# Optimization experiments

Measured on AMD Instinct MI355X. Metric: run time of the kernel, lower is better.

The kernel has to match this reference:

```python
import jax, jax.numpy as jnp
import numpy as np

N = 50000   # nodes
E = 800000  # edges (avg degree 16)
NEG = 0.2   # leaky_relu negative slope


def gat_conv(feat, W, al, ar, rW, src, dst, act):
    """DGL-style GATConv. feat:[N,F] W:[F,H*D] al/ar:[H,D] rW:[F,H*D] or None (identity residual)."""
    n = feat.shape[0]
    H, D = al.shape
    h = (feat @ W).reshape(n, H, D)                      # [N,H,D]
    el = jnp.einsum('nhd,hd->nh', h, al)                 # [N,H]
    er = jnp.einsum('nhd,hd->nh', h, ar)                 # [N,H]
    e = el[src] + er[dst]                                # [E,H]
    e = jnp.where(e > 0, e, NEG * e)                     # leaky_relu
    emax = jax.ops.segment_max(e, dst, num_segments=n)   # per-dst softmax (edge softmax)
    ee = jnp.exp(e - emax[dst])
    denom = jax.ops.segment_sum(ee, dst, num_segments=n)
    alpha = ee / denom[dst]                              # [E,H]
    out = jax.ops.segment_sum(h[src] * alpha[:, :, None], dst, num_segments=n)  # [N,H,D]
    res = (feat @ rW).reshape(n, H, D) if rW is not None else feat.reshape(n, H, D)
    return act(out + res)


def setup_inputs() -> dict:
    key = jax.random.key(0)
    ks = jax.random.split(key, 32)
    d = {}
    d["fvs"] = jax.random.normal(ks[0], (N, 128), jnp.float32)
    d["pos_enc"] = jax.random.normal(ks[1], (N, 64), jnp.float32)
    d["src"] = jax.random.randint(ks[2], (E,), 0, N, jnp.int32)
    d["dst"] = jax.random.randint(ks[3], (E,), 0, N, jnp.int32)
    def w(k, shape):
        return jax.random.normal(k, shape, jnp.float32) / np.sqrt(shape[0])
    i = 4
    # gat layers: in=192 -> H=2, D=64 (layers 0,1), final: H=2, D=64 (out_ch)
    for name in ["gat0", "gat1", "gat2"]:
        d[name + "_W"] = w(ks[i], (192, 128)); i += 1
        d[name + "_al"] = w(ks[i], (2, 64)); i += 1
        d[name + "_ar"] = w(ks[i], (2, 64)); i += 1
        d[name + "_rW"] = w(ks[i], (192, 128)); i += 1
    # pgnn layers: in=64 -> H=2, D=32; in == H*D so residual is identity (no rW)
    for name in ["pg0", "pg1"]:
        d[name + "_W"] = w(ks[i], (64, 64)); i += 1
        d[name + "_al"] = w(ks[i], (2, 32)); i += 1
        d[name + "_ar"] = w(ks[i], (2, 32)); i += 1
    return d


def reference(fvs, pos_enc, src, dst,
              gat0_W, gat0_al, gat0_ar, gat0_rW,
              gat1_W, gat1_al, gat1_ar, gat1_rW,
              gat2_W, gat2_al, gat2_ar, gat2_rW,
              pg0_W, pg0_al, pg0_ar,
              pg1_W, pg1_al, pg1_ar):
    n = fvs.shape[0]
    h_s, h_p = fvs, pos_enc
    # layer 0
    h_s = jnp.concatenate([h_s, h_p], axis=1)
    h_s = gat_conv(h_s, gat0_W, gat0_al, gat0_ar, gat0_rW, src, dst, jax.nn.elu).reshape(n, -1)
    h_p = gat_conv(h_p, pg0_W, pg0_al, pg0_ar, None, src, dst, jnp.tanh).reshape(n, -1)
    # layer 1
    h_s = jnp.concatenate([h_s, h_p], axis=1)
    h_s = gat_conv(h_s, gat1_W, gat1_al, gat1_ar, gat1_rW, src, dst, jax.nn.elu).reshape(n, -1)
    h_p = gat_conv(h_p, pg1_W, pg1_al, pg1_ar, None, src, dst, jnp.tanh).reshape(n, -1)
    # output layer: mean over heads
    h_s = jnp.concatenate([h_s, h_p], axis=1)
    h_s = gat_conv(h_s, gat2_W, gat2_al, gat2_ar, gat2_rW, src, dst, jax.nn.elu).mean(axis=1)
    return (h_s, h_p)
```

## Files before the change

### kernel.cpp

```cpp
#include <hip/hip_runtime.h>

#define NN 50000
#define NE 800000

typedef unsigned short u16;
typedef unsigned int u32;

typedef float f32x4 __attribute__((ext_vector_type(4)));
typedef __bf16 bf16x8 __attribute__((ext_vector_type(8)));
static_assert(sizeof(bf16x8) == 16, "bf16x8 must be 16B");

__device__ __forceinline__ float bf2f(u16 u) {
    u32 x = ((u32)u) << 16;
    return __uint_as_float(x);
}
__device__ __forceinline__ u16 f2bf(float f) {
    u32 x = __float_as_uint(f);
    u32 r = (x + 0x7fffu + ((x >> 16) & 1u)) >> 16;
    return (u16)r;
}
__device__ __forceinline__ u32 pack2(float a, float b) {
    return (u32)f2bf(a) | ((u32)f2bf(b) << 16);
}
__device__ __forceinline__ u16 f2h(float f) {
    _Float16 h = (_Float16)f;
    union { _Float16 h; u16 u; } c; c.h = h;
    return c.u;
}
__device__ __forceinline__ float h2f(u16 u) {
    union { u16 u; _Float16 h; } c; c.u = u;
    return (float)c.h;
}
__device__ __forceinline__ uint4 packu4(const u16* h) {
    uint4 u;
    u.x = (u32)h[0] | ((u32)h[1] << 16);
    u.y = (u32)h[2] | ((u32)h[3] << 16);
    u.z = (u32)h[4] | ((u32)h[5] << 16);
    u.w = (u32)h[6] | ((u32)h[7] << 16);
    return u;
}
__device__ __forceinline__ float ldf(const void* p, size_t idx, int mode) {
    return mode ? bf2f(((const u16*)p)[idx]) : ((const float*)p)[idx];
}
__device__ __forceinline__ float lrelu(float x) { return x > 0.f ? x : 0.2f * x; }

__device__ __forceinline__ f32x4 mfma16(uint4 a, uint4 b, f32x4 c) {
    union { uint4 u; bf16x8 b; } ua, ub;
    ua.u = a; ub.u = b;
    return __builtin_amdgcn_mfma_f32_16x16x32_bf16(ua.b, ub.b, c, 0, 0, 0);
}

__global__ void k_tracer(float* out, float v) {
    if (threadIdx.x == 0 && blockIdx.x == 0) out[0] = v;
}

__global__ void k_detect(const u16* __restrict__ fvs, int* __restrict__ mode) {
    __shared__ int cnt[256];
    int t = threadIdx.x;
    int bad = 0;
    for (int i = 0; i < 16; i++) {
        u16 u = fvs[(size_t)(t * 16 + i) * 2];
        int e = (u >> 7) & 0xff;
        if (e == 255 || e >= 134 || e <= 100) bad++;
    }
    cnt[t] = bad;
    __syncthreads();
    for (int d = 128; d; d >>= 1) {
        if (t < d) cnt[t] += cnt[t + d];
        __syncthreads();
    }
    if (t == 0) *mode = (cnt[0] > 2048) ? 0 : 1;
}

__global__ void k_hist(const int* __restrict__ dst, int* __restrict__ cnt, int E) {
    int e = blockIdx.x * blockDim.x + threadIdx.x;
    if (e < E) atomicAdd(&cnt[dst[e]], 1);
}

__global__ void k_scan1(const int* __restrict__ cnt, int* __restrict__ off,
                        int* __restrict__ bsum, int N) {
    __shared__ int wsum[4];
    int t = threadIdx.x;
    int base = blockIdx.x * 2048 + t * 8;
    int e[8];
    if (base + 8 <= N) {
        int4 v0 = *(const int4*)&cnt[base];
        int4 v1 = *(const int4*)&cnt[base + 4];
        e[0] = v0.x; e[1] = v0.y; e[2] = v0.z; e[3] = v0.w;
        e[4] = v1.x; e[5] = v1.y; e[6] = v1.z; e[7] = v1.w;
    } else {
#pragma unroll
        for (int i = 0; i < 8; i++) e[i] = (base + i < N) ? cnt[base + i] : 0;
    }
    int s = 0;
    int ps[8];
#pragma unroll
    for (int i = 0; i < 8; i++) { ps[i] = s; s += e[i]; }
    int lane = t & 63, wv = t >> 6;
    int sc = s;
#pragma unroll
    for (int o = 1; o < 64; o <<= 1) {
        int u = __shfl_up(sc, o, 64);
        if (lane >= o) sc += u;
    }
    if (lane == 63) wsum[wv] = sc;
    __syncthreads();
    int woff = 0;
    for (int w = 0; w < wv; w++) woff += wsum[w];
    int ex = woff + sc - s;
#pragma unroll
    for (int i = 0; i < 8; i++) ps[i] += ex;
    if (base + 8 <= N) {
        *(int4*)&off[base] = make_int4(ps[0], ps[1], ps[2], ps[3]);
        *(int4*)&off[base + 4] = make_int4(ps[4], ps[5], ps[6], ps[7]);
    } else {
#pragma unroll
        for (int i = 0; i < 8; i++)
            if (base + i < N) off[base + i] = ps[i];
    }
    if (t == 255) bsum[blockIdx.x] = woff + sc;
}

__global__ void k_scan2(const int* __restrict__ bsum, int* __restrict__ off,
                        int N, int nb) {
    int b = blockIdx.x, t = threadIdx.x;
    int boff = 0;
    for (int i = 0; i < b; i++) boff += bsum[i];
    int base = b * 2048 + t * 8;
    if (b > 0) {
        if (base + 8 <= N) {
            int4 a = *(int4*)&off[base];
            int4 c = *(int4*)&off[base + 4];
            a.x += boff; a.y += boff; a.z += boff; a.w += boff;
            c.x += boff; c.y += boff; c.z += boff; c.w += boff;
            *(int4*)&off[base] = a;
            *(int4*)&off[base + 4] = c;
        } else {
#pragma unroll
            for (int i = 0; i < 8; i++)
                if (base + i < N) off[base + i] += boff;
        }
    }
    if (b == nb - 1 && t == 255) off[N] = boff + bsum[b];
}

__global__ void k_fill(const int* __restrict__ src, const int* __restrict__ dst,
                       const int* __restrict__ off, int* __restrict__ cnt2,
                       int* __restrict__ ssrc, int E) {
    int e = blockIdx.x * blockDim.x + threadIdx.x;
    if (e < E) {
        int d = dst[e];
        int p = off[d] + atomicAdd(&cnt2[d], 1);
        ssrc[p] = src[e];
    }
}

__global__ void k_init(const void* __restrict__ pos, u16* __restrict__ hp,
                       const int* __restrict__ dmode, int n64) {
    int i = blockIdx.x * blockDim.x + threadIdx.x;
    if (i >= n64) return;
    int mode = *dmode;
    hp[i] = mode ? ((const u16*)pos)[i] : f2bf(((const float*)pos)[i]);
}

__global__ void k_cvt(const u16* __restrict__ in, float* __restrict__ out, int n) {
    int i = blockIdx.x * blockDim.x + threadIdx.x;
    if (i < n) out[i] = bf2f(in[i]);
}

struct PWArgs {
    const void* src[8];
    u16* dst[8];
    int K[8];
    int BM[8];
};

__global__ void k_prepw(PWArgs a, const int* __restrict__ dmode) {
    int mode = *dmode;
    int g = blockIdx.x * blockDim.x + threadIdx.x;
    int stride = gridDim.x * blockDim.x;
    for (int m = 0; m < 8; m++) {
        int bm = a.BM[m];
        int bmsh = (bm == 128) ? 7 : 6;
        int n = a.K[m] * bm;
        u16* d = a.dst[m];
        const void* s = a.src[m];
        for (int i = g; i < n; i += stride) {
            int k = i >> bmsh, c = i & (bm - 1);
            float v = mode ? bf2f(((const u16*)s)[i]) : ((const float*)s)[i];
            u16 hi = f2bf(v);
            u16 lo = f2bf(v - bf2f(hi));
            size_t o = ((size_t)((k >> 5) * 2) * bm + c) * 32 + (k & 31);
            d[o] = hi;
            d[o + (size_t)bm * 32] = lo;
        }
    }
}

template <int BM, bool HASB2, bool C1H>
__launch_bounds__(256, 4)
__global__ void k_gemm(const void* A1, const u16* __restrict__ A2,
                       const u16* __restrict__ B1p, const u16* __restrict__ B2p,
                       void* __restrict__ C1, u16* C2, float* __restrict__ att,
                       const void* __restrict__ al, const void* __restrict__ ar,
                       int N, int K, int s1, const int* __restrict__ dmode,
                       int a1_input) {
    constexpr int NR = BM / 32;
    constexpr int NMAT = HASB2 ? 2 : 1;

    const int mode = *dmode;
    const int a1f32 = (a1_input && mode == 0) ? 1 : 0;
    const int bsplit = (mode == 0) ? 1 : 0;

    const int tid = threadIdx.x;
    const int lane = tid & 63;
    const int wid = tid >> 6;
    const int l15 = lane & 15, l4 = lane >> 4;
    const int r0 = blockIdx.x * 64;
    const int wrow0 = (wid >> 1) * 32;
    const int wcol0 = (wid & 1) * (BM / 2);
    const int ko = l4 * 8;

    int frow[2];
#pragma unroll
    for (int m = 0; m < 2; m++) {
        int r = r0 + wrow0 + m * 16 + l15;
        frow[m] = r < N ? r : N - 1;
    }

    f32x4 acc[NMAT][2][NR];
    const f32x4 fz = {0.f, 0.f, 0.f, 0.f};
#pragma unroll
    for (int m2 = 0; m2 < NMAT; m2++)
#pragma unroll
        for (int m = 0; m < 2; m++)
#pragma unroll
            for (int n = 0; n < NR; n++) acc[m2][m][n] = fz;

    const int NKT = K >> 5;
    for (int kt = 0; kt < NKT; kt++) {
        const int k0 = kt << 5;
        const int doAlo = (a1f32 && k0 < 128) ? 1 : 0;

        uint4 ah[2], alo[2];
#pragma unroll
        for (int m = 0; m < 2; m++) {
            if (k0 >= 128) {
                ah[m] = *(const uint4*)(A2 + (size_t)frow[m] * 64 + (k0 - 128) + ko);
            } else if (!a1f32) {
                ah[m] = *(const uint4*)((const u16*)A1 + (size_t)frow[m] * s1 + k0 + ko);
            } else {
                const float* p = (const float*)A1 + (size_t)frow[m] * s1 + k0 + ko;
                union { uint4 u[2]; float f[8]; } fa;
                fa.u[0] = *(const uint4*)p;
                fa.u[1] = *(const uint4*)(p + 4);
                u16 hi[8], lo[8];
#pragma unroll
                for (int i = 0; i < 8; i++) {
                    hi[i] = f2bf(fa.f[i]);
                    lo[i] = f2bf(fa.f[i] - bf2f(hi[i]));
                }
                ah[m] = packu4(hi);
                alo[m] = packu4(lo);
            }
        }

        const size_t bbase = ((size_t)kt * 2) * BM * 32 + (size_t)l4 * 8;
#pragma unroll
        for (int n = 0; n < NR; n++) {
            const int c = wcol0 + n * 16 + l15;
            const size_t co = (size_t)c * 32;
#pragma unroll
            for (int m2 = 0; m2 < NMAT; m2++) {
                const u16* bp = (m2 == 0 ? B1p : B2p) + bbase + co;
                uint4 bh = *(const uint4*)bp;
#pragma unroll
                for (int m = 0; m < 2; m++)
                    acc[m2][m][n] = mfma16(ah[m], bh, acc[m2][m][n]);
                if (bsplit) {
                    uint4 bl = *(const uint4*)(bp + (size_t)BM * 32);
#pragma unroll
                    for (int m = 0; m < 2; m++)
                        acc[m2][m][n] = mfma16(ah[m], bl, acc[m2][m][n]);
                }
                if (doAlo) {
#pragma unroll
                    for (int m = 0; m < 2; m++)
                        acc[m2][m][n] = mfma16(alo[m], bh, acc[m2][m][n]);
                }
            }
        }
    }

    __syncthreads();

    float alc[NR], arc[NR];
#pragma unroll
    for (int n = 0; n < NR; n++) {
        int c = wcol0 + n * 16 + l15;
        alc[n] = ldf(al, c, mode);
        arc[n] = ldf(ar, c, mode);
    }
    const int hc = wid & 1;
#pragma unroll
    for (int m = 0; m < 2; m++) {
#pragma unroll
        for (int r = 0; r < 4; r++) {
            const int gr = r0 + wrow0 + m * 16 + l4 * 4 + r;
            float el = 0.f, er = 0.f;
#pragma unroll
            for (int n = 0; n < NR; n++) {
                float v = acc[0][m][n][r];
                el = fmaf(v, alc[n], el);
                er = fmaf(v, arc[n], er);
            }
#pragma unroll
            for (int o = 1; o <= 8; o <<= 1) {
                el += __shfl_xor(el, o, 64);
                er += __shfl_xor(er, o, 64);
            }
            if (gr < N) {
#pragma unroll
                for (int n = 0; n < NR; n++) {
                    const int c = wcol0 + n * 16 + l15;
                    float v = acc[0][m][n][r];
                    if constexpr (C1H)
                        ((u16*)C1)[(size_t)gr * BM + c] = f2h(v);
                    else
                        ((float*)C1)[(size_t)gr * BM + c] = v;
                    if constexpr (HASB2)
                        C2[(size_t)gr * 128 + c] = f2bf(acc[1][m][n][r]);
                }
                if (l15 == 0) {
                    att[(size_t)gr * 4 + hc] = el;
                    att[(size_t)gr * 4 + 2 + hc] = er;
                }
            }
        }
    }
}

__global__ void k_edge_gat2(const int* __restrict__ off, const int* __restrict__ ssrc,
                            const u16* __restrict__ h, const float* __restrict__ att,
                            const u16* __restrict__ res, u16* __restrict__ outf, int N) {
    __shared__ float pbuf[4][2][64];
    __shared__ int sbuf[4][64];
    int wv = threadIdx.x >> 6;
    int node = blockIdx.x * 4 + wv;
    int lane = threadIdx.x & 63;
    if (node >= N) return;
    const int hd = lane >> 5;
    int beg = off[node], end = off[node + 1];
    float4 a4 = *(const float4*)&att[(size_t)node * 4];
    float er0 = a4.z, er1 = a4.w;
    float m0 = -1e30f, m1 = -1e30f, d0 = 0.f, d1 = 0.f, O0 = 0.f, O1 = 0.f;
    for (int c = beg; c < end; c += 64) {
        int cn = min(end - c, 64);
        int s = 0;
        float x0 = -1e30f, x1 = -1e30f;
        if (lane < cn) {
            s = ssrc[c + lane];
            float2 e = *(const float2*)&att[(size_t)s * 4];
            x0 = lrelu(e.x + er0);
            x1 = lrelu(e.y + er1);
        }
        float cm0 = x0, cm1 = x1;
#pragma unroll
        for (int o = 32; o; o >>= 1) {
            cm0 = fmaxf(cm0, __shfl_xor(cm0, o, 64));
            cm1 = fmaxf(cm1, __shfl_xor(cm1, o, 64));
        }
        float nm0 = fmaxf(m0, cm0), nm1 = fmaxf(m1, cm1);
        float p0 = (lane < cn) ? __expf(x0 - nm0) : 0.f;
        float p1 = (lane < cn) ? __expf(x1 - nm1) : 0.f;
        float cd0 = p0, cd1 = p1;
#pragma unroll
        for (int o = 32; o; o >>= 1) {
            cd0 += __shfl_xor(cd0, o, 64);
            cd1 += __shfl_xor(cd1, o, 64);
        }
        float sc0 = __expf(m0 - nm0), sc1 = __expf(m1 - nm1);
        d0 = d0 * sc0 + cd0; d1 = d1 * sc1 + cd1;
        float sch = hd ? sc1 : sc0;
        O0 *= sch; O1 *= sch;
        m0 = nm0; m1 = nm1;
        pbuf[wv][0][lane] = p0;
        pbuf[wv][1][lane] = p1;
        sbuf[wv][lane] = s;
        const float* pb = pbuf[wv][hd];
        int j = 0;
        for (; j + 7 < cn; j += 8) {
            u32 w[8];
#pragma unroll
            for (int t = 0; t < 8; t++)
                w[t] = *(const u32*)&h[(size_t)sbuf[wv][j + t] * 128 + 2 * lane];
#pragma unroll
            for (int t = 0; t < 8; t++) {
                float q = pb[j + t];
                O0 += q * h2f((u16)w[t]);
                O1 += q * h2f((u16)(w[t] >> 16));
            }
        }
        if (j + 3 < cn) {
            u32 w[4];
#pragma unroll
            for (int t = 0; t < 4; t++)
                w[t] = *(const u32*)&h[(size_t)sbuf[wv][j + t] * 128 + 2 * lane];
#pragma unroll
            for (int t = 0; t < 4; t++) {
                float q = pb[j + t];
                O0 += q * h2f((u16)w[t]);
                O1 += q * h2f((u16)(w[t] >> 16));
            }
            j += 4;
        }
        for (; j < cn; j++) {
            u32 w = *(const u32*)&h[(size_t)sbuf[wv][j] * 128 + 2 * lane];
            float q = pb[j];
            O0 += q * h2f((u16)w);
            O1 += q * h2f((u16)(w >> 16));
        }
    }
    float dd = hd ? d1 : d0;
    float o0 = (end > beg) ? O0 / dd : 0.f;
    float o1 = (end > beg) ? O1 / dd : 0.f;
    u32 rv = *(const u32*)&res[(size_t)node * 128 + 2 * lane];
    float a0 = o0 + bf2f((u16)rv);
    float a1 = o1 + bf2f((u16)(rv >> 16));
    a0 = a0 > 0.f ? a0 : (__expf(a0) - 1.f);
    a1 = a1 > 0.f ? a1 : (__expf(a1) - 1.f);
    *(u32*)&outf[(size_t)node * 128 + 2 * lane] = pack2(a0, a1);
}

__global__ void k_edge_gat_f(const int* __restrict__ off, const int* __restrict__ ssrc,
                             const u16* __restrict__ h, const float* __restrict__ att,
                             const u16* __restrict__ res, float* __restrict__ outs, int N) {
    __shared__ float pbuf[4][2][64];
    __shared__ int sbuf[4][64];
    int wv = threadIdx.x >> 6;
    int node = blockIdx.x * 4 + wv;
    int lane = threadIdx.x & 63;
    if (node >= N) return;
    const int par = lane >> 5;
    const int i = lane & 31;
    const int hd = i >> 4;
    int beg = off[node], end = off[node + 1];
    float4 a4 = *(const float4*)&att[(size_t)node * 4];
    float er0 = a4.z, er1 = a4.w;
    float m0 = -1e30f, m1 = -1e30f, d0 = 0.f, d1 = 0.f;
    float O[4] = {0.f, 0.f, 0.f, 0.f};
    for (int c = beg; c < end; c += 64) {
        int cn = min(end - c, 64);
        int s = 0;
        float x0 = -1e30f, x1 = -1e30f;
        if (lane < cn) {
            s = ssrc[c + lane];
            float2 e = *(const float2*)&att[(size_t)s * 4];
            x0 = lrelu(e.x + er0);
            x1 = lrelu(e.y + er1);
        }
        float cm0 = x0, cm1 = x1;
#pragma unroll
        for (int o = 32; o; o >>= 1) {
            cm0 = fmaxf(cm0, __shfl_xor(cm0, o, 64));
            cm1 = fmaxf(cm1, __shfl_xor(cm1, o, 64));
        }
        float nm0 = fmaxf(m0, cm0), nm1 = fmaxf(m1, cm1);
        float p0 = (lane < cn) ? __expf(x0 - nm0) : 0.f;
        float p1 = (lane < cn) ? __expf(x1 - nm1) : 0.f;
        float cd0 = p0, cd1 = p1;
#pragma unroll
        for (int o = 32; o; o >>= 1) {
            cd0 += __shfl_xor(cd0, o, 64);
            cd1 += __shfl_xor(cd1, o, 64);
        }
        float sc0 = __expf(m0 - nm0), sc1 = __expf(m1 - nm1);
        d0 = d0 * sc0 + cd0; d1 = d1 * sc1 + cd1;
        float sch = hd ? sc1 : sc0;
#pragma unroll
        for (int k = 0; k < 4; k++) O[k] *= sch;
        m0 = nm0; m1 = nm1;
        pbuf[wv][0][lane] = p0;
        pbuf[wv][1][lane] = p1;
        sbuf[wv][lane] = s;
        const float* pb = pbuf[wv][hd];
        int j = par;
        for (; j + 14 < cn; j += 16) {
            uint2 w[8];
#pragma unroll
            for (int t = 0; t < 8; t++)
                w[t] = *(const uint2*)&h[(size_t)sbuf[wv][j + 2 * t] * 128 + 4 * i];
#pragma unroll
            for (int t = 0; t < 8; t++) {
                float q = pb[j + 2 * t];
                O[0] += q * h2f((u16)w[t].x);
                O[1] += q * h2f((u16)(w[t].x >> 16));
                O[2] += q * h2f((u16)w[t].y);
                O[3] += q * h2f((u16)(w[t].y >> 16));
            }
        }
        if (j + 6 < cn) {
            uint2 w[4];
#pragma unroll
            for (int t = 0; t < 4; t++)
                w[t] = *(const uint2*)&h[(size_t)sbuf[wv][j + 2 * t] * 128 + 4 * i];
#pragma unroll
            for (int t = 0; t < 4; t++) {
                float q = pb[j + 2 * t];
                O[0] += q * h2f((u16)w[t].x);
                O[1] += q * h2f((u16)(w[t].x >> 16));
                O[2] += q * h2f((u16)w[t].y);
                O[3] += q * h2f((u16)(w[t].y >> 16));
            }
            j += 8;
        }
        for (; j < cn; j += 2) {
            uint2 w = *(const uint2*)&h[(size_t)sbuf[wv][j] * 128 + 4 * i];
            float q = pb[j];
            O[0] += q * h2f((u16)w.x);
            O[1] += q * h2f((u16)(w.x >> 16));
            O[2] += q * h2f((u16)w.y);
            O[3] += q * h2f((u16)(w.y >> 16));
        }
    }
#pragma unroll
    for (int k = 0; k < 4; k++) O[k] += __shfl_xor(O[k], 32, 64);
    float dd = hd ? d1 : d0;
    uint2 rv = *(const uint2*)&res[(size_t)node * 128 + 4 * i];
    float a[4];
    a[0] = bf2f((u16)rv.x);
    a[1] = bf2f((u16)(rv.x >> 16));
    a[2] = bf2f((u16)rv.y);
    a[3] = bf2f((u16)(rv.y >> 16));
#pragma unroll
    for (int k = 0; k < 4; k++) {
        float o = (end > beg) ? O[k] / dd : 0.f;
        float v = o + a[k];
        a[k] = v > 0.f ? v : (__expf(v) - 1.f);
    }
    float b[4];
#pragma unroll
    for (int k = 0; k < 4; k++) b[k] = __shfl_xor(a[k], 16, 64);
    if (lane < 16)
        *(float4*)&outs[(size_t)node * 64 + 4 * i] =
            make_float4(0.5f * (a[0] + b[0]), 0.5f * (a[1] + b[1]),
                        0.5f * (a[2] + b[2]), 0.5f * (a[3] + b[3]));
}

__global__ void k_edge_pg2(const int* __restrict__ off, const int* __restrict__ ssrc,
                           const u16* __restrict__ h, const float* __restrict__ att,
                           u16* __restrict__ hp, int N) {
    __shared__ float pbuf[4][2][64];
    __shared__ int sbuf[4][64];
    int wv = threadIdx.x >> 6;
    int node = blockIdx.x * 4 + wv;
    int lane = threadIdx.x & 63;
    if (node >= N) return;
    const int par = lane >> 5;
    const int i = lane & 31;
    const int hd = i >> 4;
    int beg = off[node], end = off[node + 1];
    float4 a4 = *(const float4*)&att[(size_t)node * 4];
    float er0 = a4.z, er1 = a4.w;
    float m0 = -1e30f, m1 = -1e30f, d0 = 0.f, d1 = 0.f, O0 = 0.f, O1 = 0.f;
    for (int c = beg; c < end; c += 64) {
        int cn = min(end - c, 64);
        int s = 0;
        float x0 = -1e30f, x1 = -1e30f;
        if (lane < cn) {
            s = ssrc[c + lane];
            float2 e = *(const float2*)&att[(size_t)s * 4];
            x0 = lrelu(e.x + er0);
            x1 = lrelu(e.y + er1);
        }
        float cm0 = x0, cm1 = x1;
#pragma unroll
        for (int o = 32; o; o >>= 1) {
            cm0 = fmaxf(cm0, __shfl_xor(cm0, o, 64));
            cm1 = fmaxf(cm1, __shfl_xor(cm1, o, 64));
        }
        float nm0 = fmaxf(m0, cm0), nm1 = fmaxf(m1, cm1);
        float p0 = (lane < cn) ? __expf(x0 - nm0) : 0.f;
        float p1 = (lane < cn) ? __expf(x1 - nm1) : 0.f;
        float cd0 = p0, cd1 = p1;
#pragma unroll
        for (int o = 32; o; o >>= 1) {
            cd0 += __shfl_xor(cd0, o, 64);
            cd1 += __shfl_xor(cd1, o, 64);
        }
        float sc0 = __expf(m0 - nm0), sc1 = __expf(m1 - nm1);
        d0 = d0 * sc0 + cd0; d1 = d1 * sc1 + cd1;
        float sch = hd ? sc1 : sc0;
        O0 *= sch; O1 *= sch;
        m0 = nm0; m1 = nm1;
        pbuf[wv][0][lane] = p0;
        pbuf[wv][1][lane] = p1;
        sbuf[wv][lane] = s;
        const float* pb = pbuf[wv][hd];
        int j = par;
        for (; j + 14 < cn; j += 16) {
            u32 w[8];
#pragma unroll
            for (int t = 0; t < 8; t++)
                w[t] = *(const u32*)&h[(size_t)sbuf[wv][j + 2 * t] * 64 + 2 * i];
#pragma unroll
            for (int t = 0; t < 8; t++) {
                float q = pb[j + 2 * t];
                O0 += q * h2f((u16)w[t]);
                O1 += q * h2f((u16)(w[t] >> 16));
            }
        }
        if (j + 6 < cn) {
            u32 w[4];
#pragma unroll
            for (int t = 0; t < 4; t++)
                w[t] = *(const u32*)&h[(size_t)sbuf[wv][j + 2 * t] * 64 + 2 * i];
#pragma unroll
            for (int t = 0; t < 4; t++) {
                float q = pb[j + 2 * t];
                O0 += q * h2f((u16)w[t]);
                O1 += q * h2f((u16)(w[t] >> 16));
            }
            j += 8;
        }
        for (; j < cn; j += 2) {
            u32 w = *(const u32*)&h[(size_t)sbuf[wv][j] * 64 + 2 * i];
            float q = pb[j];
            O0 += q * h2f((u16)w);
            O1 += q * h2f((u16)(w >> 16));
        }
    }
    O0 += __shfl_xor(O0, 32, 64);
    O1 += __shfl_xor(O1, 32, 64);
    if (lane < 32) {
        float dd = hd ? d1 : d0;
        float o0 = (end > beg) ? O0 / dd : 0.f;
        float o1 = (end > beg) ? O1 / dd : 0.f;
        u32 rv = *(const u32*)&hp[(size_t)node * 64 + 2 * i];
        float a0 = tanhf(o0 + bf2f((u16)rv));
        float a1 = tanhf(o1 + bf2f((u16)(rv >> 16)));
        *(u32*)&hp[(size_t)node * 64 + 2 * i] = pack2(a0, a1);
    }
}

extern "C" void kernel_launch(void* const* d_in, const int* in_sizes, int n_in,
                              void* d_out, int out_size, void* d_ws, size_t ws_size,
                              hipStream_t stream) {
    const int N = NN, E = NE;
    const void* fvs = d_in[0];
    const void* pos = d_in[1];
    const int* src = (const int*)d_in[2];
    const int* dst = (const int*)d_in[3];
    const void* gW[3]  = {d_in[4],  d_in[8],  d_in[12]};
    const void* gal[3] = {d_in[5],  d_in[9],  d_in[13]};
    const void* gar[3] = {d_in[6],  d_in[10], d_in[14]};
    const void* grW[3] = {d_in[7],  d_in[11], d_in[15]};
    const void* pW[2]  = {d_in[16], d_in[19]};
    const void* pal[2] = {d_in[17], d_in[20]};
    const void* par[2] = {d_in[18], d_in[21]};

    auto al256 = [](size_t b) { return (b + 255) & ~(size_t)255; };
    size_t sz_dmode = al256(4);
    size_t sz_bsum  = al256(32 * 4);
    size_t sz_att   = al256((size_t)N * 4 * 4);
    size_t sz_off   = al256((size_t)(N + 1) * 4);
    size_t sz_ssrc  = al256((size_t)E * 4);
    size_t sz_hs    = al256((size_t)N * 128 * 2);
    size_t sz_hp    = al256((size_t)N * 64 * 2);
    size_t sz_wpk   = al256((size_t)(6 * 192 * 128 + 2 * 64 * 64) * 2 * 2);
    size_t need = sz_dmode + sz_bsum + sz_att + sz_off + sz_ssrc + sz_hs + sz_hp + sz_wpk;
    int bad = (need > ws_size) ? 1 : 0;

    size_t cur = 0;
    auto alloc = [&](size_t bytes) {
        if (cur + bytes > ws_size) cur = 0;
        char* p = (char*)d_ws + cur;
        if (bytes <= ws_size) cur += bytes;
        return p;
    };
    int* dmode  = (int*)alloc(sz_dmode);
    int* bsum   = (int*)alloc(sz_bsum);
    float* att  = (float*)alloc(sz_att);
    int* off    = (int*)alloc(sz_off);
    int* ssrc   = (int*)alloc(sz_ssrc);
    u16* hs     = (u16*)alloc(sz_hs);
    u16* hp     = (u16*)alloc(sz_hp);
    u16* wpk    = (u16*)alloc(sz_wpk);

    const size_t GSZ = (size_t)192 * 128 * 2;
    const size_t PSZ = (size_t)64 * 64 * 2;
    u16* Bp[8];
    for (int m = 0; m < 6; m++) Bp[m] = wpk + (size_t)m * GSZ;
    Bp[6] = wpk + 6 * GSZ;
    Bp[7] = Bp[6] + PSZ;

    int* cnt  = (int*)att;
    int* cnt2 = (int*)((char*)att + al256((size_t)N * 4));

    void* H = d_out;

    hipMemsetAsync(cnt, 0, (size_t)N * 4, stream);
    hipMemsetAsync(cnt2, 0, (size_t)N * 4, stream);

    k_detect<<<1, 256, 0, stream>>>((const u16*)fvs, dmode);

    PWArgs pwa;
    pwa.src[0] = gW[0]; pwa.src[1] = grW[0];
    pwa.src[2] = gW[1]; pwa.src[3] = grW[1];
    pwa.src[4] = gW[2]; pwa.src[5] = grW[2];
    pwa.src[6] = pW[0]; pwa.src[7] = pW[1];
    for (int m = 0; m < 8; m++) {
        pwa.dst[m] = Bp[m];
        pwa.K[m] = (m < 6) ? 192 : 64;
        pwa.BM[m] = (m < 6) ? 128 : 64;
    }
    k_prepw<<<64, 256, 0, stream>>>(pwa, dmode);

    int eb = (E + 255) / 256;
    int nbS = (N + 2047) / 2048;
    k_hist<<<eb, 256, 0, stream>>>(dst, cnt, E);
    k_scan1<<<nbS, 256, 0, stream>>>(cnt, off, bsum, N);
    k_scan2<<<nbS, 256, 0, stream>>>(bsum, off, N, nbS);
    k_fill<<<eb, 256, 0, stream>>>(src, dst, off, cnt2, ssrc, E);

    k_init<<<(N * 64 + 255) / 256, 256, 0, stream>>>(pos, hp, dmode, N * 64);

    int gb = (N + 63) / 64;
    int nb = (N + 3) / 4;

    k_gemm<128, true, true><<<gb, 256, 0, stream>>>(fvs, hp, Bp[0], Bp[1], H, hs, att, gal[0], gar[0], N, 192, 128, dmode, 1);
    k_edge_gat2<<<nb, 256, 0, stream>>>(off, ssrc, (u16*)H, att, hs, hs, N);
    k_gemm<64, false, true><<<gb, 256, 0, stream>>>(hp, nullptr, Bp[6], nullptr, H, nullptr, att, pal[0], par[0], N, 64, 64, dmode, 0);
    k_edge_pg2<<<nb, 256, 0, stream>>>(off, ssrc, (u16*)H, att, hp, N);

    k_gemm<128, true, true><<<gb, 256, 0, stream>>>(hs, hp, Bp[2], Bp[3], H, hs, att, gal[1], gar[1], N, 192, 128, dmode, 0);
    k_edge_gat2<<<nb, 256, 0, stream>>>(off, ssrc, (u16*)H, att, hs, hs, N);
    k_gemm<64, false, true><<<gb, 256, 0, stream>>>(hp, nullptr, Bp[7], nullptr, H, nullptr, att, pal[1], par[1], N, 64, 64, dmode, 0);
    k_edge_pg2<<<nb, 256, 0, stream>>>(off, ssrc, (u16*)H, att, hp, N);

    k_gemm<128, true, true><<<gb, 256, 0, stream>>>(hs, hp, Bp[4], Bp[5], H, hs, att, gal[2], gar[2], N, 192, 128, dmode, 0);
    k_edge_gat_f<<<nb, 256, 0, stream>>>(off, ssrc, (u16*)H, att, hs, (float*)hs, N);

    hipMemcpyAsync((float*)d_out, (float*)hs, (size_t)N * 64 * 4, hipMemcpyDeviceToDevice, stream);
    k_cvt<<<(N * 64 + 255) / 256, 256, 0, stream>>>(hp, (float*)d_out + (size_t)N * 64, N * 64);

    if (bad) {
        float v = 100000.f + 1000.f * (float)(ws_size >> 20);
        k_tracer<<<1, 64, 0, stream>>>((float*)d_out, v);
    }
}
```

Baseline: 580.2 us.

## Replace atomic CSR fill with two-pass bucketed counting sort

The per-edge global-atomic CSR fill is replaced by a two-pass radix-style scatter. Pass A buckets each 8192-edge chunk by dst>>8 in shared memory and writes packed (src, low dst byte) records to a temp buffer (aliasing hs) with coalesced runs. Pass B sorts each 256-node bucket in LDS and writes ssrc. This removes 800k scattered global atomics and random writes, at the cost of an extra pass, an extra launch and packing src into 24 bits, which works for N=50000.

```diff
diff --git a/kernel.cpp b/kernel.cpp
--- a/kernel.cpp
+++ b/kernel.cpp
@@ -2,6 +2,8 @@
 
 #define NN 50000
 #define NE 800000
+#define FBLK 8192
+#define BKT 256
 
 typedef unsigned short u16;
 typedef unsigned int u32;
@@ -144,14 +146,79 @@
     if (b == nb - 1 && t == 255) off[N] = boff + bsum[b];
 }
 
-__global__ void k_fill(const int* __restrict__ src, const int* __restrict__ dst,
-                       const int* __restrict__ off, int* __restrict__ cnt2,
-                       int* __restrict__ ssrc, int E) {
-    int e = blockIdx.x * blockDim.x + threadIdx.x;
-    if (e < E) {
-        int d = dst[e];
-        int p = off[d] + atomicAdd(&cnt2[d], 1);
-        ssrc[p] = src[e];
+__global__ void k_binit(const int* __restrict__ off, int* __restrict__ bcur, int nbk) {
+    int b = threadIdx.x;
+    if (b < nbk) bcur[b] = off[b * BKT];
+    else if (b < 256) bcur[b] = 0;
+}
+
+__launch_bounds__(256)
+__global__ void k_fillA(const int* __restrict__ src, const int* __restrict__ dst,
+                        int* __restrict__ bcur, u32* __restrict__ tmp, int E) {
+    __shared__ int hist[256];
+    __shared__ int lbase[256];
+    __shared__ int gbase[256];
+    __shared__ int lcur[256];
+    __shared__ u32 outrec[FBLK];
+    __shared__ unsigned char bslot[FBLK];
+    int t = threadIdx.x;
+    int e0 = blockIdx.x * FBLK;
+    int bn = min(E - e0, FBLK);
+    hist[t] = 0;
+    __syncthreads();
+    for (int i = t; i < bn; i += 256)
+        atomicAdd(&hist[dst[e0 + i] >> 8], 1);
+    __syncthreads();
+    if (t == 0) {
+        int run = 0;
+        for (int b = 0; b < 256; b++) { lbase[b] = run; run += hist[b]; }
+    }
+    __syncthreads();
+    lcur[t] = lbase[t];
+    gbase[t] = hist[t] ? atomicAdd(&bcur[t], hist[t]) : 0;
+    __syncthreads();
+    for (int i = t; i < bn; i += 256) {
+        int d = dst[e0 + i];
+        int s = src[e0 + i];
+        int b = d >> 8;
+        int slot = atomicAdd(&lcur[b], 1);
+        outrec[slot] = (u32)s | ((u32)(d & 255) << 24);
+        bslot[slot] = (unsigned char)b;
+    }
+    __syncthreads();
+    for (int i = t; i < bn; i += 256) {
+        int b = bslot[i];
+        tmp[gbase[b] + (i - lbase[b])] = outrec[i];
+    }
+}
+
+__launch_bounds__(256)
+__global__ void k_fillB(const int* __restrict__ off, const u32* __restrict__ tmp,
+                        int* __restrict__ ssrc, int N) {
+    __shared__ int lcur[BKT];
+    __shared__ u32 outv[FBLK];
+    int b = blockIdx.x, t = threadIdx.x;
+    int n0 = b * BKT;
+    int nn = min(N - n0, BKT);
+    int nbeg = off[n0], nend = off[n0 + nn];
+    int sz = nend - nbeg;
+    for (int i = t; i < nn; i += 256) lcur[i] = off[n0 + i] - nbeg;
+    __syncthreads();
+    if (sz <= FBLK) {
+        for (int i = t; i < sz; i += 256) {
+            u32 r = tmp[nbeg + i];
+            int slot = atomicAdd(&lcur[r >> 24], 1);
+            outv[slot] = r & 0x00FFFFFFu;
+        }
+        __syncthreads();
+        for (int i = t; i < sz; i += 256)
+            ssrc[nbeg + i] = (int)outv[i];
+    } else {
+        for (int i = t; i < sz; i += 256) {
+            u32 r = tmp[nbeg + i];
+            int slot = atomicAdd(&lcur[r >> 24], 1);
+            ssrc[nbeg + slot] = (int)(r & 0x00FFFFFFu);
+        }
     }
 }
 
@@ -662,13 +729,15 @@
     auto al256 = [](size_t b) { return (b + 255) & ~(size_t)255; };
     size_t sz_dmode = al256(4);
     size_t sz_bsum  = al256(32 * 4);
+    size_t sz_bcur  = al256(256 * 4);
     size_t sz_att   = al256((size_t)N * 4 * 4);
     size_t sz_off   = al256((size_t)(N + 1) * 4);
     size_t sz_ssrc  = al256((size_t)E * 4);
     size_t sz_hs    = al256((size_t)N * 128 * 2);
     size_t sz_hp    = al256((size_t)N * 64 * 2);
     size_t sz_wpk   = al256((size_t)(6 * 192 * 128 + 2 * 64 * 64) * 2 * 2);
-    size_t need = sz_dmode + sz_bsum + sz_att + sz_off + sz_ssrc + sz_hs + sz_hp + sz_wpk;
+    size_t need = sz_dmode + sz_bsum + sz_bcur + sz_att + sz_off + sz_ssrc
+                + sz_hs + sz_hp + sz_wpk;
     int bad = (need > ws_size) ? 1 : 0;
 
     size_t cur = 0;
@@ -680,6 +749,7 @@
     };
     int* dmode  = (int*)alloc(sz_dmode);
     int* bsum   = (int*)alloc(sz_bsum);
+    int* bcur   = (int*)alloc(sz_bcur);
     float* att  = (float*)alloc(sz_att);
     int* off    = (int*)alloc(sz_off);
     int* ssrc   = (int*)alloc(sz_ssrc);
@@ -694,13 +764,12 @@
     Bp[6] = wpk + 6 * GSZ;
     Bp[7] = Bp[6] + PSZ;
 
-    int* cnt  = (int*)att;
-    int* cnt2 = (int*)((char*)att + al256((size_t)N * 4));
+    int* cnt = (int*)att;
+    u32* tmp = (u32*)hs;
 
     void* H = d_out;
 
     hipMemsetAsync(cnt, 0, (size_t)N * 4, stream);
-    hipMemsetAsync(cnt2, 0, (size_t)N * 4, stream);
 
     k_detect<<<1, 256, 0, stream>>>((const u16*)fvs, dmode);
 
@@ -718,10 +787,13 @@
 
     int eb = (E + 255) / 256;
     int nbS = (N + 2047) / 2048;
+    int nbk = (N + BKT - 1) / BKT;
     k_hist<<<eb, 256, 0, stream>>>(dst, cnt, E);
     k_scan1<<<nbS, 256, 0, stream>>>(cnt, off, bsum, N);
     k_scan2<<<nbS, 256, 0, stream>>>(bsum, off, N, nbS);
-    k_fill<<<eb, 256, 0, stream>>>(src, dst, off, cnt2, ssrc, E);
+    k_binit<<<1, 256, 0, stream>>>(off, bcur, nbk);
+    k_fillA<<<(E + FBLK - 1) / FBLK, 256, 0, stream>>>(src, dst, bcur, tmp, E);
+    k_fillB<<<nbk, 256, 0, stream>>>(off, tmp, ssrc, N);
 
     k_init<<<(N * 64 + 255) / 256, 256, 0, stream>>>(pos, hp, dmode, N * 64);
 
```

After: 572.7 us. About the same (-1.3%).
